# Optimization experiments

Hardware: AMD Instinct MI355X
Metric: run time of the kernel (lower is better)

## Reference

```python
import jax, jax.numpy as jnp
import numpy as np

B, H = 4096, 1024
N1, N2, N3 = 28, 280, 2800  # nodes (== classes == paths) per level, branching [28,10,10]


def setup_inputs() -> dict:
    key = jax.random.key(0)
    ks = jax.random.split(key, 8)
    s = 1.0 / np.sqrt(H)  # torch nn.Linear default init bound
    x = jax.random.normal(ks[0], (B, H), jnp.float32)
    labels = jax.random.randint(ks[1], (B,), 0, N3, dtype=jnp.int32)
    W1 = jax.random.uniform(ks[2], (N1, H), jnp.float32, -s, s)
    b1 = jax.random.uniform(ks[3], (N1,), jnp.float32, -s, s)
    W2 = jax.random.uniform(ks[4], (N2, H), jnp.float32, -s, s)
    b2 = jax.random.uniform(ks[5], (N2,), jnp.float32, -s, s)
    W3 = jax.random.uniform(ks[6], (N3, H), jnp.float32, -s, s)
    b3 = jax.random.uniform(ks[7], (N3,), jnp.float32, -s, s)
    return {"x": x, "labels": labels, "W1": W1, "b1": b1,
            "W2": W2, "b2": b2, "W3": W3, "b3": b3}


def _ce(logits, lab):
    # mean cross-entropy, same as torch.nn.CrossEntropyLoss (mean reduction)
    lp = jax.nn.log_softmax(logits, axis=-1)
    return -jnp.take_along_axis(lp, lab[:, None], axis=1).mean()


def reference(x, labels, W1, b1, W2, b2, W3, b3):
    # per-level node probabilities: one grouped GEMM per level replaces the
    # Python loop of tiny Linear(hidden,1)+sigmoid calls
    z1 = jax.nn.sigmoid(x @ W1.T + b1)  # [B, N1]
    z2 = jax.nn.sigmoid(x @ W2.T + b2)  # [B, N2]
    z3 = jax.nn.sigmoid(x @ W3.T + b3)  # [B, N3]

    # path (prefix) matrices: leaf k has path [k//100, k//10, k].
    # NOTE: all nodes of a path index into the CURRENT level's weights,
    # exactly as self.nodes[lvl][node] does in the source.
    i2 = jnp.arange(N2)
    p2 = jnp.stack([i2 // 10, i2], axis=1)                    # [N2, 2]
    i3 = jnp.arange(N3)
    p3 = jnp.stack([i3 // 100, i3 // 10, i3], axis=1)          # [N3, 3]

    logits1 = z1                                               # prod over length-1 path
    logits2 = jnp.prod(z2[:, p2], axis=-1)                     # [B, N2]
    logits3 = jnp.prod(z3[:, p3], axis=-1)                     # [B, N3]

    # update_label_per_lvl: label -> ancestor node id at that level
    lab1 = labels // 100
    lab2 = labels // 10
    loss = _ce(logits1, lab1) + _ce(logits2, lab2) + _ce(logits3, labels)
    return logits3, loss
```

## Files before the change

### kernel.cpp

```cpp
#include <hip/hip_runtime.h>
#include <cstdint>


typedef unsigned short u16;
typedef unsigned char u8;
typedef long i64;
typedef float f32x4 __attribute__((ext_vector_type(4)));

#define AS_G __attribute__((address_space(1)))
#define AS_L __attribute__((address_space(3)))

constexpr int BATCH = 4096;
constexpr int H     = 1024;
constexpr int N1 = 28, N2 = 280, N3 = 2800;
constexpr int NT = N1 + N2 + N3;
constexpr int NP = 3200;
constexpr int NANC = N1 + N2 + 280;
constexpr float WSCALE = 16.0f;
constexpr float WINV   = 1.0f / 16.0f;

__device__ inline u16 f2bf(float f) {
    unsigned int u = __float_as_uint(f);
    u += 0x7fffu + ((u >> 16) & 1u);
    return (u16)(u >> 16);
}
__device__ inline float bf2f(unsigned int u) { return __uint_as_float(u << 16); }

__device__ inline unsigned int pk4_fp8(float a, float b, float c, float d) {
    unsigned int r = __builtin_amdgcn_cvt_pk_fp8_f32(a, b, 0, false);
    r = __builtin_amdgcn_cvt_pk_fp8_f32(c, d, (int)r, true);
    return r;
}

constexpr int XG = (BATCH * H) / 4;
constexpr int WG = (NP * H) / 4;
constexpr int BG = NP / 4;

__global__ __launch_bounds__(256) void cast_kernel(
        const float* __restrict__ x,
        const float* __restrict__ W1, const float* __restrict__ W2,
        const float* __restrict__ W3,
        const float* __restrict__ b1, const float* __restrict__ b2,
        const float* __restrict__ b3,
        u8* __restrict__ Xq, u8* __restrict__ Wq, float* __restrict__ biasf) {
    int g = blockIdx.x * 256 + threadIdx.x;
    if (g < XG) {
        float4 v = ((const float4*)x)[g];
        ((unsigned int*)Xq)[g] = pk4_fp8(v.x, v.y, v.z, v.w);
    } else if (g < XG + WG) {
        int wg = g - XG;
        int row = wg >> 8, cg = wg & 255;
        float4 v = make_float4(0.f, 0.f, 0.f, 0.f);
        if (row < N1)           v = ((const float4*)W1)[row * 256 + cg];
        else if (row < N1 + N2) v = ((const float4*)W2)[(row - N1) * 256 + cg];
        else if (row < NT)      v = ((const float4*)W3)[(row - N1 - N2) * 256 + cg];
        ((unsigned int*)Wq)[wg] = pk4_fp8(v.x * WSCALE, v.y * WSCALE, v.z * WSCALE, v.w * WSCALE);
    } else if (g < XG + WG + BG) {
        int bg = g - XG - WG;
        float4 v; float* vp = &v.x;
        #pragma unroll
        for (int i = 0; i < 4; ++i) {
            int c = bg * 4 + i; float t = 0.f;
            if (c < N1)           t = b1[c];
            else if (c < N1 + N2) t = b2[c - N1];
            else if (c < NT)      t = b3[c - N1 - N2];
            vp[i] = t;
        }
        ((float4*)biasf)[bg] = v;
    }
}

__global__ __launch_bounds__(256) void gemm_sig(
        const u8* __restrict__ Xq, const u8* __restrict__ Wq,
        const float* __restrict__ biasf, u16* __restrict__ Zb) {
    __shared__ __align__(16) u8 As[2][2 * 64 * 32];
    __shared__ __align__(16) u8 Bs[2][2 * 128 * 32];

    const int id  = blockIdx.x;
    const int xcd = id & 7;
    const int j   = id >> 3;
    const int m0 = ((xcd << 3) | (j & 7)) * 64;
    const int n0 = (j >> 3) * 128;

    const int tid  = threadIdx.x;
    const int lane = tid & 63;
    const int wave = tid >> 6;
    const int wr = wave >> 1;
    const int wc = wave & 1;

    const int laneM = lane & 15;
    const int u   = lane >> 4;
    const int xb  = (laneM >> 2) & 1;
    const int laneKb = (((u >> 1) ^ xb) << 4) + (u & 1) * 8;

    const int ac = tid;
    const int apanel = ac >> 7, arem = ac & 127;
    const int arowi = arem >> 1, av = arem & 1;
    const int agoff = apanel * 32 + ((av ^ ((arowi >> 2) & 1)) << 4);
    int brow[2], bgoff[2];
    #pragma unroll
    for (int t = 0; t < 2; ++t) {
        const int c = tid + 256 * t;
        const int panel = c >> 8, rem = c & 255;
        const int row = rem >> 1, v = rem & 1;
        brow[t]  = row;
        bgoff[t] = panel * 32 + ((v ^ ((row >> 2) & 1)) << 4);
    }

    auto STAGE = [&](int bufi, int kt) {
        const int k0 = kt * 64;
        __builtin_amdgcn_global_load_lds(
            (const AS_G uint32_t*)(Xq + (size_t)(m0 + arowi) * H + k0 + agoff),
            (AS_L uint32_t*)&As[bufi][ac * 16], 16, 0, 0);
        #pragma unroll
        for (int t = 0; t < 2; ++t) {
            const int c = tid + 256 * t;
            __builtin_amdgcn_global_load_lds(
                (const AS_G uint32_t*)(Wq + (size_t)(n0 + brow[t]) * H + k0 + bgoff[t]),
                (AS_L uint32_t*)&Bs[bufi][c * 16], 16, 0, 0);
        }
    };

    f32x4 acc[2][4] = {};

    STAGE(0, 0);
    __syncthreads();
    int buf = 0;
    for (int kt = 0; kt < H / 64; ++kt) {
        if (kt + 1 < H / 64) STAGE(buf ^ 1, kt + 1);
        #pragma unroll
        for (int p = 0; p < 2; ++p) {
            i64 af[2], bfv[4];
            #pragma unroll
            for (int i = 0; i < 2; ++i)
                af[i]  = *(const i64*)&As[buf][p * 2048 + (wr * 32 + i * 16 + laneM) * 32 + laneKb];
            #pragma unroll
            for (int i = 0; i < 4; ++i)
                bfv[i] = *(const i64*)&Bs[buf][p * 4096 + (wc * 64 + i * 16 + laneM) * 32 + laneKb];
            #pragma unroll
            for (int am = 0; am < 2; ++am)
                #pragma unroll
                for (int bn = 0; bn < 4; ++bn)
                    acc[am][bn] = __builtin_amdgcn_mfma_f32_16x16x32_fp8_fp8(
                        af[am], bfv[bn], acc[am][bn], 0, 0, 0);
        }
        __syncthreads();
        buf ^= 1;
    }

    #pragma unroll
    for (int bn = 0; bn < 4; ++bn) {
        const int col = n0 + wc * 64 + bn * 16 + laneM;
        if (col >= NT) continue;
        const float bias = biasf[col];
        #pragma unroll
        for (int am = 0; am < 2; ++am) {
            const int rbase = m0 + wr * 32 + am * 16 + (lane >> 4) * 4;
            #pragma unroll
            for (int r = 0; r < 4; ++r) {
                float v = acc[am][bn][r] * WINV + bias;
                Zb[(size_t)(rbase + r) * NP + col] = f2bf(1.0f / (1.0f + __expf(-v)));
            }
        }
    }
}

__global__ __launch_bounds__(256) void logits_loss(
        const u16* __restrict__ Zb, const int* __restrict__ labels,
        float* __restrict__ out, float* __restrict__ partials) {
    __shared__ float zs[NANC];
    __shared__ float red[12];
    const int b = blockIdx.x, tid = threadIdx.x;
    const u16* Zrow = Zb + (size_t)b * NP;

    const unsigned int* Zr = (const unsigned int*)Zrow;
    for (int i = tid; i < NANC / 2; i += 256) {
        unsigned int v = Zr[i];
        zs[2 * i]     = bf2f(v & 0xffffu);
        zs[2 * i + 1] = bf2f(v >> 16);
    }
    __syncthreads();

    float se1 = 0.f, se2 = 0.f, se3 = 0.f;
    float4* outr4 = (float4*)(out + (size_t)b * N3);
    const uint2* Z3s = (const uint2*)(Zrow + N1 + N2);
    for (int q = tid; q < N3 / 4; q += 256) {
        const uint2 zv = Z3s[q];
        float z3v[4] = { bf2f(zv.x & 0xffffu), bf2f(zv.x >> 16),
                         bf2f(zv.y & 0xffffu), bf2f(zv.y >> 16) };
        const int k = q * 4;
        float4 o; float* op = &o.x;
        #pragma unroll
        for (int uu = 0; uu < 4; ++uu) {
            const int kk = k + uu;
            float lg = z3v[uu] * zs[308 + kk / 10] * zs[308 + kk / 100];
            op[uu] = lg;
            se3 += __expf(lg);
        }
        outr4[q] = o;
    }
    for (int jj = tid; jj < N2; jj += 256)
        se2 += __expf(zs[N1 + jj] * zs[N1 + jj / 10]);
    if (tid < N1)
        se1 = __expf(zs[tid]);

    #pragma unroll
    for (int off = 32; off > 0; off >>= 1) {
        se1 += __shfl_down(se1, off, 64);
        se2 += __shfl_down(se2, off, 64);
        se3 += __shfl_down(se3, off, 64);
    }
    if ((tid & 63) == 0) {
        int w = tid >> 6;
        red[w] = se3; red[4 + w] = se2; red[8 + w] = se1;
    }
    __syncthreads();
    if (tid == 0) {
        float s3 = red[0] + red[1] + red[2] + red[3];
        float s2 = red[4] + red[5] + red[6] + red[7];
        float s1 = red[8] + red[9] + red[10] + red[11];
        int lab  = labels[b];
        int lab2 = lab / 10, lab1 = lab / 100;
        float l1 = zs[lab1];
        float l2 = zs[N1 + lab2] * zs[N1 + lab2 / 10];
        float l3 = bf2f((unsigned int)Zrow[N1 + N2 + lab]) * zs[308 + lab2] * zs[308 + lab1];
        partials[b] = (logf(s1) - l1) + (logf(s2) - l2) + (logf(s3) - l3);
    }
}

__global__ __launch_bounds__(256) void final_reduce(
        const float* __restrict__ partials, float* __restrict__ out) {
    __shared__ float red[4];
    const int tid = threadIdx.x;
    float s = 0.f;
    for (int i = tid; i < BATCH; i += 256) s += partials[i];
    #pragma unroll
    for (int off = 32; off > 0; off >>= 1) s += __shfl_down(s, off, 64);
    if ((tid & 63) == 0) red[tid >> 6] = s;
    __syncthreads();
    if (tid == 0)
        out[(size_t)BATCH * N3] = (red[0] + red[1] + red[2] + red[3]) * (1.0f / BATCH);
}

extern "C" void kernel_launch(void* const* d_in, const int* in_sizes, int n_in,
                              void* d_out, int out_size, void* d_ws, size_t ws_size,
                              hipStream_t stream) {
    const float* x      = (const float*)d_in[0];
    const int*   labels = (const int*)d_in[1];
    const float* W1     = (const float*)d_in[2];
    const float* b1     = (const float*)d_in[3];
    const float* W2     = (const float*)d_in[4];
    const float* b2     = (const float*)d_in[5];
    const float* W3     = (const float*)d_in[6];
    const float* b3     = (const float*)d_in[7];
    float* out = (float*)d_out;

    char* ws = (char*)d_ws;
    u8*    Xq       = (u8*)ws;
    u8*    Wq       = (u8*)(ws + 4194304);
    u16*   Zb       = (u16*)(ws + 7471104);
    float* biasf    = (float*)(ws + 33685504);
    float* partials = (float*)(ws + 33698304);

    cast_kernel<<<(XG + WG + BG + 255) / 256, 256, 0, stream>>>(
        x, W1, W2, W3, b1, b2, b3, Xq, Wq, biasf);
    gemm_sig<<<1600, 256, 0, stream>>>(Xq, Wq, biasf, Zb);
    logits_loss<<<BATCH, 256, 0, stream>>>(Zb, labels, out, partials);
    final_reduce<<<1, 256, 0, stream>>>(partials, out);
}
```

Measured before the change: 149.4 us.

## Load GEMM fragments directly from global memory, dropping LDS double buffering

The FP8 GEMM no longer stages X and W tiles through double-buffered shared memory with global_load_lds and barriers. Each lane now reads its 8-byte MFMA fragments straight from global memory every k-step, with the loop unrolled by 4. This removes the LDS traffic and __syncthreads, but loses the cooperative reuse of tiles across waves and issues many small uncoalesced 8-byte global loads, so performance now depends on L1/L2 hit rates.

Result: slower. 263.9 us (+76.7%).

```diff
diff --git a/kernel.cpp b/kernel.cpp
--- a/kernel.cpp
+++ b/kernel.cpp
@@ -6,9 +6,6 @@
 typedef unsigned char u8;
 typedef long i64;
 typedef float f32x4 __attribute__((ext_vector_type(4)));
-
-#define AS_G __attribute__((address_space(1)))
-#define AS_L __attribute__((address_space(3)))
 
 constexpr int BATCH = 4096;
 constexpr int H     = 1024;
@@ -73,9 +70,6 @@
 __global__ __launch_bounds__(256) void gemm_sig(
         const u8* __restrict__ Xq, const u8* __restrict__ Wq,
         const float* __restrict__ biasf, u16* __restrict__ Zb) {
-    __shared__ __align__(16) u8 As[2][2 * 64 * 32];
-    __shared__ __align__(16) u8 Bs[2][2 * 128 * 32];
-
     const int id  = blockIdx.x;
     const int xcd = id & 7;
     const int j   = id >> 3;
@@ -89,63 +83,34 @@
     const int wc = wave & 1;
 
     const int laneM = lane & 15;
-    const int u   = lane >> 4;
-    const int xb  = (laneM >> 2) & 1;
-    const int laneKb = (((u >> 1) ^ xb) << 4) + (u & 1) * 8;
-
-    const int ac = tid;
-    const int apanel = ac >> 7, arem = ac & 127;
-    const int arowi = arem >> 1, av = arem & 1;
-    const int agoff = apanel * 32 + ((av ^ ((arowi >> 2) & 1)) << 4);
-    int brow[2], bgoff[2];
-    #pragma unroll
-    for (int t = 0; t < 2; ++t) {
-        const int c = tid + 256 * t;
-        const int panel = c >> 8, rem = c & 255;
-        const int row = rem >> 1, v = rem & 1;
-        brow[t]  = row;
-        bgoff[t] = panel * 32 + ((v ^ ((row >> 2) & 1)) << 4);
-    }
-
-    auto STAGE = [&](int bufi, int kt) {
-        const int k0 = kt * 64;
-        __builtin_amdgcn_global_load_lds(
-            (const AS_G uint32_t*)(Xq + (size_t)(m0 + arowi) * H + k0 + agoff),
-            (AS_L uint32_t*)&As[bufi][ac * 16], 16, 0, 0);
-        #pragma unroll
-        for (int t = 0; t < 2; ++t) {
-            const int c = tid + 256 * t;
-            __builtin_amdgcn_global_load_lds(
-                (const AS_G uint32_t*)(Wq + (size_t)(n0 + brow[t]) * H + k0 + bgoff[t]),
-                (AS_L uint32_t*)&Bs[bufi][c * 16], 16, 0, 0);
-        }
-    };
+    const int u     = lane >> 4;
+
+    unsigned offA[2], offB[4];
+    #pragma unroll
+    for (int i = 0; i < 2; ++i)
+        offA[i] = (unsigned)(m0 + wr * 32 + i * 16 + laneM) * H + u * 8;
+    #pragma unroll
+    for (int i = 0; i < 4; ++i)
+        offB[i] = (unsigned)(n0 + wc * 64 + i * 16 + laneM) * H + u * 8;
 
     f32x4 acc[2][4] = {};
 
-    STAGE(0, 0);
-    __syncthreads();
-    int buf = 0;
-    for (int kt = 0; kt < H / 64; ++kt) {
-        if (kt + 1 < H / 64) STAGE(buf ^ 1, kt + 1);
-        #pragma unroll
-        for (int p = 0; p < 2; ++p) {
-            i64 af[2], bfv[4];
+    #pragma unroll 4
+    for (int kt = 0; kt < H / 32; ++kt) {
+        const int kb = kt * 32;
+        i64 af[2], bfv[4];
+        #pragma unroll
+        for (int i = 0; i < 2; ++i)
+            af[i]  = *(const i64*)(Xq + offA[i] + kb);
+        #pragma unroll
+        for (int i = 0; i < 4; ++i)
+            bfv[i] = *(const i64*)(Wq + offB[i] + kb);
+        #pragma unroll
+        for (int am = 0; am < 2; ++am)
             #pragma unroll
-            for (int i = 0; i < 2; ++i)
-                af[i]  = *(const i64*)&As[buf][p * 2048 + (wr * 32 + i * 16 + laneM) * 32 + laneKb];
-            #pragma unroll
-            for (int i = 0; i < 4; ++i)
-                bfv[i] = *(const i64*)&Bs[buf][p * 4096 + (wc * 64 + i * 16 + laneM) * 32 + laneKb];
-            #pragma unroll
-            for (int am = 0; am < 2; ++am)
-                #pragma unroll
-                for (int bn = 0; bn < 4; ++bn)
-                    acc[am][bn] = __builtin_amdgcn_mfma_f32_16x16x32_fp8_fp8(
-                        af[am], bfv[bn], acc[am][bn], 0, 0, 0);
-        }
-        __syncthreads();
-        buf ^= 1;
+            for (int bn = 0; bn < 4; ++bn)
+                acc[am][bn] = __builtin_amdgcn_mfma_f32_16x16x32_fp8_fp8(
+                    af[am], bfv[bn], acc[am][bn], 0, 0, 0);
     }
 
     #pragma unroll
@@ -155,7 +120,7 @@
         const float bias = biasf[col];
         #pragma unroll
         for (int am = 0; am < 2; ++am) {
-            const int rbase = m0 + wr * 32 + am * 16 + (lane >> 4) * 4;
+            const int rbase = m0 + wr * 32 + am * 16 + u * 4;
             #pragma unroll
             for (int r = 0; r < 4; ++r) {
                 float v = acc[am][bn][r] * WINV + bias;
```
